# Kernel optimization log

Hardware: AMD Instinct MI355X
Metric: run time of the kernel (lower is better)

## Reference

```python
import jax, jax.numpy as jnp
import numpy as np

DIM = 1024
N_HEADS = 16
HEAD_DIM = DIM // N_HEADS
MLP = 4 * DIM
B, N = 2, 2048
LN_EPS = 1e-5


def setup_inputs() -> dict:
    key = jax.random.key(0)
    ks = jax.random.split(key, 12)
    s = lambda fan_in: 1.0 / np.sqrt(fan_in)
    return {
        "x": jax.random.normal(ks[0], (B, N, DIM), dtype=jnp.float32),
        "qkv_w": jax.random.uniform(ks[1], (3 * DIM, DIM), jnp.float32, -s(DIM), s(DIM)),
        "out_w": jax.random.uniform(ks[2], (DIM, DIM), jnp.float32, -s(DIM), s(DIM)),
        "out_b": jax.random.uniform(ks[3], (DIM,), jnp.float32, -s(DIM), s(DIM)),
        "ff_w1": jax.random.uniform(ks[4], (MLP, DIM), jnp.float32, -s(DIM), s(DIM)),
        "ff_b1": jax.random.uniform(ks[5], (MLP,), jnp.float32, -s(DIM), s(DIM)),
        "ff_w2": jax.random.uniform(ks[6], (DIM, MLP), jnp.float32, -s(MLP), s(MLP)),
        "ff_b2": jax.random.uniform(ks[7], (DIM,), jnp.float32, -s(MLP), s(MLP)),
        "ln1_w": jnp.ones((DIM,), jnp.float32),
        "ln1_b": jnp.zeros((DIM,), jnp.float32),
        "ln2_w": jnp.ones((DIM,), jnp.float32),
        "ln2_b": jnp.zeros((DIM,), jnp.float32),
    }


def _layernorm(x, w, b):
    mu = jnp.mean(x, axis=-1, keepdims=True)
    var = jnp.mean(jnp.square(x - mu), axis=-1, keepdims=True)
    return (x - mu) * jax.lax.rsqrt(var + LN_EPS) * w + b


def reference(x, qkv_w, out_w, out_b, ff_w1, ff_b1, ff_w2, ff_b2,
              ln1_w, ln1_b, ln2_w, ln2_b):
    Bx, Nx, D = x.shape
    scale = HEAD_DIM ** -0.5
    x_ln = _layernorm(x, ln1_w, ln1_b)
    qkv = (x_ln @ qkv_w.T).reshape(Bx, Nx, 3, N_HEADS, HEAD_DIM)
    qkv = jnp.transpose(qkv, (2, 0, 3, 1, 4))  # [3, B, H, N, hd]
    q, k, v = qkv[0], qkv[1], qkv[2]
    attn = jnp.einsum('bhid,bhjd->bhij', q, k) * scale
    attn = jax.nn.softmax(attn, axis=-1)
    o = jnp.einsum('bhij,bhjd->bhid', attn, v)
    o = jnp.transpose(o, (0, 2, 1, 3)).reshape(Bx, Nx, D)
    x = x + o @ out_w.T + out_b
    x_ln2 = _layernorm(x, ln2_w, ln2_b)
    h = jax.nn.silu(x_ln2 @ ff_w1.T + ff_b1)
    x = x + h @ ff_w2.T + ff_b2
    return x
```

## Files before the change

### kernel.cpp

```cpp
#include <hip/hip_runtime.h>
#include <stdint.h>

#define DIM   1024
#define NH    16
#define HD    64
#define SEQ   2048
#define BATCH 2
#define MROWS 4096
#define MLPD  4096
#define LN_EPS 1e-5f
#define QSCALE 0.18033688011112042f

typedef _Float16 f16;
typedef _Float16 half8 __attribute__((ext_vector_type(8)));
typedef _Float16 half4 __attribute__((ext_vector_type(4)));
typedef float f32x4 __attribute__((ext_vector_type(4)));

__device__ __forceinline__ void async_cp16(const void* g, void* l) {
  __builtin_amdgcn_global_load_lds(
      (const __attribute__((address_space(1))) unsigned int*)g,
      (__attribute__((address_space(3))) unsigned int*)l, 16, 0, 0);
}

__global__ __launch_bounds__(256) void cvt_all_kernel(
    const float* __restrict__ w0, const float* __restrict__ w1,
    const float* __restrict__ w2, const float* __restrict__ w3,
    f16* __restrict__ d0, f16* __restrict__ d1, f16* __restrict__ d2,
    f16* __restrict__ d3) {
  int blk = blockIdx.x;
  const float* s;
  f16* d;
  int base;
  if (blk < 3072)      { s = w0; d = d0; base = blk; }
  else if (blk < 4096) { s = w1; d = d1; base = blk - 3072; }
  else if (blk < 8192) { s = w2; d = d2; base = blk - 4096; }
  else                 { s = w3; d = d3; base = blk - 8192; }
  int i = (base * 256 + threadIdx.x) * 4;
  float4 v = *(const float4*)(s + i);
  half4 o = { (f16)v.x, (f16)v.y, (f16)v.z, (f16)v.w };
  *(half4*)(d + i) = o;
}

__global__ __launch_bounds__(256) void ln_kernel(const float* __restrict__ x,
    const float* __restrict__ w, const float* __restrict__ b, f16* __restrict__ out) {
  __shared__ float red[8];
  int row = blockIdx.x, t = threadIdx.x;
  const float4 v = ((const float4*)(x + (size_t)row * DIM))[t];
  float s1 = v.x + v.y + v.z + v.w;
  float s2 = v.x * v.x + v.y * v.y + v.z * v.z + v.w * v.w;
#pragma unroll
  for (int m = 32; m; m >>= 1) { s1 += __shfl_xor(s1, m); s2 += __shfl_xor(s2, m); }
  if ((t & 63) == 0) { red[t >> 6] = s1; red[4 + (t >> 6)] = s2; }
  __syncthreads();
  s1 = red[0] + red[1] + red[2] + red[3];
  s2 = red[4] + red[5] + red[6] + red[7];
  float mu = s1 * (1.f / DIM);
  float rs = rsqrtf(s2 * (1.f / DIM) - mu * mu + LN_EPS);
  float4 wv = ((const float4*)w)[t];
  float4 bv = ((const float4*)b)[t];
  half4 o = { (f16)((v.x - mu) * rs * wv.x + bv.x), (f16)((v.y - mu) * rs * wv.y + bv.y),
              (f16)((v.z - mu) * rs * wv.z + bv.z), (f16)((v.w - mu) * rs * wv.w + bv.w) };
  ((half4*)(out + (size_t)row * DIM))[t] = o;
}

template <int MODE, int TN>
__global__ __launch_bounds__(256) void gemm_bt(
    const f16* __restrict__ A, const f16* __restrict__ W,
    const float* __restrict__ bias, const float* __restrict__ resid,
    float* __restrict__ outf, f16* __restrict__ outq, f16* __restrict__ outk,
    f16* __restrict__ outv, int K) {
  constexpr int IT = (TN == 128) ? 4 : 2;
  constexpr int MSUB = IT * 16;
  __shared__ __align__(16) f16 As[128 * 64];
  __shared__ __align__(16) f16 Bs[TN * 64];
  const int t = threadIdx.x;
  const int wave = t >> 6, lane = t & 63;
  const int n16 = lane & 15, quad = lane >> 4;
  const int tile_m = blockIdx.y * 128, tile_n = blockIdx.x * TN;
  const int wm = (TN == 128) ? (wave >> 1) : wave;
  const int wn = (TN == 128) ? (wave & 1) : 0;
  const int srow = lane >> 3, spos = lane & 7;
  const f32x4 zero4 = {0.f, 0.f, 0.f, 0.f};

  f32x4 acc[IT][4];
#pragma unroll
  for (int i = 0; i < IT; i++)
#pragma unroll
    for (int j = 0; j < 4; j++) acc[i][j] = zero4;

  for (int k0 = 0; k0 < K; k0 += 64) {
#pragma unroll
    for (int q = 0; q < 4; q++) {
      int r = q * 32 + wave * 8 + srow;
      int c = spos ^ (r & 7);
      async_cp16(A + (size_t)(tile_m + r) * K + k0 + c * 8, &As[q * 2048 + wave * 512]);
    }
#pragma unroll
    for (int q = 0; q < TN / 32; q++) {
      int r = q * 32 + wave * 8 + srow;
      int c = spos ^ (r & 7);
      async_cp16(W + (size_t)(tile_n + r) * K + k0 + c * 8, &Bs[q * 2048 + wave * 512]);
    }
    __syncthreads();
#pragma unroll
    for (int kk = 0; kk < 2; kk++) {
      half8 af[IT], bfr[4];
#pragma unroll
      for (int i = 0; i < IT; i++) {
        int row = wm * MSUB + i * 16 + n16;
        int c = (kk * 4 + quad) ^ (row & 7);
        af[i] = *(const half8*)&As[row * 64 + c * 8];
      }
#pragma unroll
      for (int j = 0; j < 4; j++) {
        int row = wn * 64 + j * 16 + n16;
        int c = (kk * 4 + quad) ^ (row & 7);
        bfr[j] = *(const half8*)&Bs[row * 64 + c * 8];
      }
#pragma unroll
      for (int i = 0; i < IT; i++)
#pragma unroll
        for (int j = 0; j < 4; j++)
          acc[i][j] = __builtin_amdgcn_mfma_f32_16x16x32_f16(af[i], bfr[j], acc[i][j], 0, 0, 0);
    }
    __syncthreads();
  }

#pragma unroll
  for (int i = 0; i < IT; i++) {
#pragma unroll
    for (int j = 0; j < 4; j++) {
      int gcol = tile_n + wn * 64 + j * 16 + n16;
      int grow0 = tile_m + wm * MSUB + i * 16 + quad * 4;
      if constexpr (MODE == 0) {
        int tsel = gcol >> 10, h = (gcol >> 6) & 15, d = gcol & 63;
        int bb = grow0 >> 11, nn0 = grow0 & 2047;
        if (tsel == 2) {
          half4 o;
#pragma unroll
          for (int r = 0; r < 4; r++) o[r] = (f16)acc[i][j][r];
          *(half4*)&outv[(((size_t)bb * NH + h) * HD + d) * SEQ + nn0] = o;
        } else {
          f16* dst = (tsel == 0) ? outq : outk;
          float sc = (tsel == 0) ? QSCALE : 1.0f;
#pragma unroll
          for (int r = 0; r < 4; r++)
            dst[(((size_t)bb * NH + h) * SEQ + nn0 + r) * HD + d] = (f16)(acc[i][j][r] * sc);
        }
      } else if constexpr (MODE == 1) {
#pragma unroll
        for (int r = 0; r < 4; r++) {
          size_t idx = (size_t)(grow0 + r) * DIM + gcol;
          outf[idx] = acc[i][j][r] + bias[gcol] + resid[idx];
        }
      } else {
#pragma unroll
        for (int r = 0; r < 4; r++) {
          float z = acc[i][j][r] + bias[gcol];
          float sg = 1.f / (1.f + __expf(-z));
          outq[(size_t)(grow0 + r) * MLPD + gcol] = (f16)(z * sg);
        }
      }
    }
  }
}

__global__ __launch_bounds__(256, 4) void attn_kernel(const f16* __restrict__ qg,
    const f16* __restrict__ kg, const f16* __restrict__ vtg,
    float* __restrict__ op, float* __restrict__ lp) {
  __shared__ __align__(16) f16 Ks[64 * 64];
  __shared__ __align__(16) f16 Vs[64 * 64];
  const int bh = blockIdx.z, kc = blockIdx.y, q0 = blockIdx.x * 128;
  const int t = threadIdx.x, wave = t >> 6, lane = t & 63;
  const int n16 = lane & 15, quad = lane >> 4;
  const int srow = lane >> 3, spos = lane & 7;
  const f32x4 zero4 = {0.f, 0.f, 0.f, 0.f};

  half8 qf[2][2];
#pragma unroll
  for (int qt = 0; qt < 2; qt++) {
    const f16* qr = qg + ((size_t)bh * SEQ + q0 + wave * 32 + qt * 16 + n16) * HD + quad * 8;
    qf[qt][0] = *(const half8*)qr;
    qf[qt][1] = *(const half8*)(qr + 32);
  }

  f32x4 oc[2][4];
#pragma unroll
  for (int qt = 0; qt < 2; qt++)
#pragma unroll
    for (int dt = 0; dt < 4; dt++) oc[qt][dt] = zero4;
  float ls[2] = {0.f, 0.f};

  for (int kt64 = 0; kt64 < 16; kt64++) {
    const int kv0 = kc * 1024 + kt64 * 64;
#pragma unroll
    for (int p = 0; p < 2; p++) {
      int r = p * 32 + wave * 8 + srow;
      int c = spos ^ (r & 7);
      async_cp16(kg + ((size_t)bh * SEQ + kv0 + r) * HD + c * 8, &Ks[p * 2048 + wave * 512]);
      async_cp16(vtg + ((size_t)bh * HD + r) * SEQ + kv0 + c * 8, &Vs[p * 2048 + wave * 512]);
    }
    __syncthreads();

    f32x4 st[4][2];
#pragma unroll
    for (int kt = 0; kt < 4; kt++) {
      int row = kt * 16 + n16;
      half8 kf0 = *(const half8*)&Ks[row * 64 + (quad ^ (row & 7)) * 8];
      half8 kf1 = *(const half8*)&Ks[row * 64 + ((quad + 4) ^ (row & 7)) * 8];
#pragma unroll
      for (int qt = 0; qt < 2; qt++) {
        f32x4 z = zero4;
        z = __builtin_amdgcn_mfma_f32_16x16x32_f16(kf0, qf[qt][0], z, 0, 0, 0);
        z = __builtin_amdgcn_mfma_f32_16x16x32_f16(kf1, qf[qt][1], z, 0, 0, 0);
        st[kt][qt] = z;
      }
    }

    half4 pf[2][4];
#pragma unroll
    for (int qt = 0; qt < 2; qt++)
#pragma unroll
      for (int kt = 0; kt < 4; kt++) {
        half4 p4;
        float s0 = __builtin_exp2f(st[kt][qt][0]);
        float s1 = __builtin_exp2f(st[kt][qt][1]);
        float s2 = __builtin_exp2f(st[kt][qt][2]);
        float s3 = __builtin_exp2f(st[kt][qt][3]);
        p4[0] = (f16)s0; p4[1] = (f16)s1; p4[2] = (f16)s2; p4[3] = (f16)s3;
        ls[qt] += (s0 + s1) + (s2 + s3);
        pf[qt][kt] = p4;
      }

#pragma unroll
    for (int kt = 0; kt < 4; kt++) {
      half4 va[4];
#pragma unroll
      for (int dt = 0; dt < 4; dt++) {
        int row = dt * 16 + n16;
        int phys = (kt * 2 + (quad >> 1)) ^ (row & 7);
        va[dt] = *(const half4*)&Vs[row * 64 + phys * 8 + (quad & 1) * 4];
      }
#pragma unroll
      for (int dt = 0; dt < 4; dt++)
#pragma unroll
        for (int qt = 0; qt < 2; qt++)
          oc[qt][dt] = __builtin_amdgcn_mfma_f32_16x16x16f16(va[dt], pf[qt][kt], oc[qt][dt], 0, 0, 0);
    }
    __syncthreads();
  }

  const int b = bh >> 4, h = bh & 15;
#pragma unroll
  for (int qt = 0; qt < 2; qt++) {
    float l = ls[qt];
    l += __shfl_xor(l, 16);
    l += __shfl_xor(l, 32);
    int q = q0 + wave * 32 + qt * 16 + n16;
    int row = b * SEQ + q;
#pragma unroll
    for (int dt = 0; dt < 4; dt++)
      *(f32x4*)&op[((size_t)kc * MROWS + row) * DIM + h * HD + dt * 16 + quad * 4] = oc[qt][dt];
    if (quad == 0) lp[((size_t)kc * BATCH * NH + bh) * SEQ + q] = l;
  }
}

__global__ __launch_bounds__(256) void attn_reduce_kernel(const float* __restrict__ op,
    const float* __restrict__ lp, f16* __restrict__ obuf) {
  int row = blockIdx.x;
  int t = threadIdx.x;
  int b = row >> 11, q = row & 2047;
  int h = t >> 4;
  size_t base = (size_t)row * DIM + t * 4;
  float4 o1 = *(const float4*)&op[base];
  float4 o2 = *(const float4*)&op[(size_t)MROWS * DIM + base];
  size_t li = ((size_t)b * NH + h) * SEQ + q;
  float l = lp[li] + lp[(size_t)BATCH * NH * SEQ + li];
  float inv = 1.f / l;
  half4 o = { (f16)((o1.x + o2.x) * inv), (f16)((o1.y + o2.y) * inv),
              (f16)((o1.z + o2.z) * inv), (f16)((o1.w + o2.w) * inv) };
  *(half4*)&obuf[base] = o;
}

extern "C" void kernel_launch(void* const* d_in, const int* in_sizes, int n_in,
                              void* d_out, int out_size, void* d_ws, size_t ws_size,
                              hipStream_t stream) {
  const float* x     = (const float*)d_in[0];
  const float* qkv_w = (const float*)d_in[1];
  const float* out_w = (const float*)d_in[2];
  const float* out_b = (const float*)d_in[3];
  const float* ff_w1 = (const float*)d_in[4];
  const float* ff_b1 = (const float*)d_in[5];
  const float* ff_w2 = (const float*)d_in[6];
  const float* ff_b2 = (const float*)d_in[7];
  const float* ln1_w = (const float*)d_in[8];
  const float* ln1_b = (const float*)d_in[9];
  const float* ln2_w = (const float*)d_in[10];
  const float* ln2_b = (const float*)d_in[11];
  float* out = (float*)d_out;

  char* p = (char*)d_ws;
  size_t off = 0;
  auto alloc = [&](size_t bytes) {
    void* r = p + off;
    off += (bytes + 255) & ~(size_t)255;
    return r;
  };
  f16* wqkv = (f16*)alloc((size_t)3 * DIM * DIM * 2);
  f16* wout = (f16*)alloc((size_t)DIM * DIM * 2);
  f16* wf1  = (f16*)alloc((size_t)MLPD * DIM * 2);
  f16* wf2  = (f16*)alloc((size_t)MLPD * DIM * 2);
  f16* xln  = (f16*)alloc((size_t)MROWS * DIM * 2);
  f16* qb   = (f16*)alloc((size_t)MROWS * DIM * 2);
  f16* kb   = (f16*)alloc((size_t)MROWS * DIM * 2);
  f16* vtb  = (f16*)alloc((size_t)MROWS * DIM * 2);
  f16* obuf = (f16*)alloc((size_t)MROWS * DIM * 2);
  float* x1 = (float*)alloc((size_t)MROWS * DIM * 4);
  f16* hbuf = (f16*)alloc((size_t)MROWS * MLPD * 2);
  float* lp = (float*)alloc((size_t)2 * BATCH * NH * SEQ * 4);
  f16* x1ln = xln;
  float* op = (float*)hbuf;

  cvt_all_kernel<<<12288, 256, 0, stream>>>(qkv_w, out_w, ff_w1, ff_w2,
                                            wqkv, wout, wf1, wf2);
  ln_kernel<<<MROWS, 256, 0, stream>>>(x, ln1_w, ln1_b, xln);
  gemm_bt<0, 128><<<dim3(3 * DIM / 128, MROWS / 128), 256, 0, stream>>>(
      xln, wqkv, nullptr, nullptr, nullptr, qb, kb, vtb, DIM);
  attn_kernel<<<dim3(SEQ / 128, 2, BATCH * NH), 256, 0, stream>>>(qb, kb, vtb, op, lp);
  attn_reduce_kernel<<<MROWS, 256, 0, stream>>>(op, lp, obuf);
  gemm_bt<1, 64><<<dim3(DIM / 64, MROWS / 128), 256, 0, stream>>>(
      obuf, wout, out_b, x, x1, nullptr, nullptr, nullptr, DIM);
  ln_kernel<<<MROWS, 256, 0, stream>>>(x1, ln2_w, ln2_b, x1ln);
  gemm_bt<2, 128><<<dim3(MLPD / 128, MROWS / 128), 256, 0, stream>>>(
      x1ln, wf1, ff_b1, nullptr, nullptr, hbuf, nullptr, nullptr, DIM);
  gemm_bt<1, 64><<<dim3(DIM / 64, MROWS / 128), 256, 0, stream>>>(
      hbuf, wf2, ff_b2, x1, out, nullptr, nullptr, nullptr, MLPD);
}
```

Baseline: 364.5 us.

## Split-K the N=1024 GEMMs and fuse bias/residual/LN2 into combine kernels

The out-projection and FF2 GEMMs are split along K into two halves via a third grid dimension, writing fp32 partials into reused scratch buffers. New combine kernels sum the partials with bias and residual, and the first also computes LayerNorm2, replacing the separate LN kernel. This doubles the block count for the narrow GEMMs to fill more CUs, at the cost of extra fp32 partial traffic and an added launch. Launch bounds for TN=64 request higher occupancy.

```diff
diff --git a/kernel.cpp b/kernel.cpp
--- a/kernel.cpp
+++ b/kernel.cpp
@@ -64,11 +64,11 @@
 }
 
 template <int MODE, int TN>
-__global__ __launch_bounds__(256) void gemm_bt(
+__global__ __launch_bounds__(256, (TN == 64) ? 4 : 1) void gemm_bt(
     const f16* __restrict__ A, const f16* __restrict__ W,
-    const float* __restrict__ bias, const float* __restrict__ resid,
-    float* __restrict__ outf, f16* __restrict__ outq, f16* __restrict__ outk,
-    f16* __restrict__ outv, int K) {
+    const float* __restrict__ bias, float* __restrict__ outf,
+    f16* __restrict__ outq, f16* __restrict__ outk, f16* __restrict__ outv,
+    int K) {
   constexpr int IT = (TN == 128) ? 4 : 2;
   constexpr int MSUB = IT * 16;
   __shared__ __align__(16) f16 As[128 * 64];
@@ -82,13 +82,20 @@
   const int srow = lane >> 3, spos = lane & 7;
   const f32x4 zero4 = {0.f, 0.f, 0.f, 0.f};
 
+  int kbeg = 0, kend = K;
+  if constexpr (MODE == 3) {
+    int kc = K >> 1;
+    kbeg = blockIdx.z * kc;
+    kend = kbeg + kc;
+  }
+
   f32x4 acc[IT][4];
 #pragma unroll
   for (int i = 0; i < IT; i++)
 #pragma unroll
     for (int j = 0; j < 4; j++) acc[i][j] = zero4;
 
-  for (int k0 = 0; k0 < K; k0 += 64) {
+  for (int k0 = kbeg; k0 < kend; k0 += 64) {
 #pragma unroll
     for (int q = 0; q < 4; q++) {
       int r = q * 32 + wave * 8 + srow;
@@ -147,12 +154,10 @@
           for (int r = 0; r < 4; r++)
             dst[(((size_t)bb * NH + h) * SEQ + nn0 + r) * HD + d] = (f16)(acc[i][j][r] * sc);
         }
-      } else if constexpr (MODE == 1) {
-#pragma unroll
-        for (int r = 0; r < 4; r++) {
-          size_t idx = (size_t)(grow0 + r) * DIM + gcol;
-          outf[idx] = acc[i][j][r] + bias[gcol] + resid[idx];
-        }
+      } else if constexpr (MODE == 3) {
+        size_t base = ((size_t)blockIdx.z * MROWS + grow0) * DIM + gcol;
+#pragma unroll
+        for (int r = 0; r < 4; r++) outf[base + (size_t)r * DIM] = acc[i][j][r];
       } else {
 #pragma unroll
         for (int r = 0; r < 4; r++) {
@@ -163,6 +168,51 @@
       }
     }
   }
+}
+
+__global__ __launch_bounds__(256) void combine_ln_kernel(const float* __restrict__ op,
+    const float* __restrict__ bias, const float* __restrict__ resid,
+    const float* __restrict__ lnw, const float* __restrict__ lnb,
+    float* __restrict__ x1, f16* __restrict__ x1ln) {
+  __shared__ float red[8];
+  int row = blockIdx.x, t = threadIdx.x;
+  size_t base = (size_t)row * DIM;
+  float4 p0 = ((const float4*)&op[base])[t];
+  float4 p1 = ((const float4*)&op[(size_t)MROWS * DIM + base])[t];
+  float4 bv = ((const float4*)bias)[t];
+  float4 rv = ((const float4*)&resid[base])[t];
+  float4 v = { p0.x + p1.x + bv.x + rv.x, p0.y + p1.y + bv.y + rv.y,
+               p0.z + p1.z + bv.z + rv.z, p0.w + p1.w + bv.w + rv.w };
+  ((float4*)&x1[base])[t] = v;
+  float s1 = v.x + v.y + v.z + v.w;
+  float s2 = v.x * v.x + v.y * v.y + v.z * v.z + v.w * v.w;
+#pragma unroll
+  for (int m = 32; m; m >>= 1) { s1 += __shfl_xor(s1, m); s2 += __shfl_xor(s2, m); }
+  if ((t & 63) == 0) { red[t >> 6] = s1; red[4 + (t >> 6)] = s2; }
+  __syncthreads();
+  s1 = red[0] + red[1] + red[2] + red[3];
+  s2 = red[4] + red[5] + red[6] + red[7];
+  float mu = s1 * (1.f / DIM);
+  float rs = rsqrtf(s2 * (1.f / DIM) - mu * mu + LN_EPS);
+  float4 wv = ((const float4*)lnw)[t];
+  float4 lb = ((const float4*)lnb)[t];
+  half4 o = { (f16)((v.x - mu) * rs * wv.x + lb.x), (f16)((v.y - mu) * rs * wv.y + lb.y),
+              (f16)((v.z - mu) * rs * wv.z + lb.z), (f16)((v.w - mu) * rs * wv.w + lb.w) };
+  ((half4*)&x1ln[base])[t] = o;
+}
+
+__global__ __launch_bounds__(256) void combine_out_kernel(const float* __restrict__ op,
+    const float* __restrict__ bias, const float* __restrict__ resid,
+    float* __restrict__ out) {
+  int row = blockIdx.x, t = threadIdx.x;
+  size_t base = (size_t)row * DIM;
+  float4 p0 = ((const float4*)&op[base])[t];
+  float4 p1 = ((const float4*)&op[(size_t)MROWS * DIM + base])[t];
+  float4 bv = ((const float4*)bias)[t];
+  float4 rv = ((const float4*)&resid[base])[t];
+  float4 v = { p0.x + p1.x + bv.x + rv.x, p0.y + p1.y + bv.y + rv.y,
+               p0.z + p1.z + bv.z + rv.z, p0.w + p1.w + bv.w + rv.w };
+  ((float4*)&out[base])[t] = v;
 }
 
 __global__ __launch_bounds__(256, 4) void attn_kernel(const f16* __restrict__ qg,
@@ -319,20 +369,23 @@
   f16* hbuf = (f16*)alloc((size_t)MROWS * MLPD * 2);
   float* lp = (float*)alloc((size_t)2 * BATCH * NH * SEQ * 4);
   f16* x1ln = xln;
-  float* op = (float*)hbuf;
+  float* opa = (float*)hbuf;
+  float* op1 = (float*)hbuf;
+  float* op2 = (float*)qb;
 
   cvt_all_kernel<<<12288, 256, 0, stream>>>(qkv_w, out_w, ff_w1, ff_w2,
                                             wqkv, wout, wf1, wf2);
   ln_kernel<<<MROWS, 256, 0, stream>>>(x, ln1_w, ln1_b, xln);
   gemm_bt<0, 128><<<dim3(3 * DIM / 128, MROWS / 128), 256, 0, stream>>>(
-      xln, wqkv, nullptr, nullptr, nullptr, qb, kb, vtb, DIM);
-  attn_kernel<<<dim3(SEQ / 128, 2, BATCH * NH), 256, 0, stream>>>(qb, kb, vtb, op, lp);
-  attn_reduce_kernel<<<MROWS, 256, 0, stream>>>(op, lp, obuf);
-  gemm_bt<1, 64><<<dim3(DIM / 64, MROWS / 128), 256, 0, stream>>>(
-      obuf, wout, out_b, x, x1, nullptr, nullptr, nullptr, DIM);
-  ln_kernel<<<MROWS, 256, 0, stream>>>(x1, ln2_w, ln2_b, x1ln);
+      xln, wqkv, nullptr, nullptr, qb, kb, vtb, DIM);
+  attn_kernel<<<dim3(SEQ / 128, 2, BATCH * NH), 256, 0, stream>>>(qb, kb, vtb, opa, lp);
+  attn_reduce_kernel<<<MROWS, 256, 0, stream>>>(opa, lp, obuf);
+  gemm_bt<3, 64><<<dim3(DIM / 64, MROWS / 128, 2), 256, 0, stream>>>(
+      obuf, wout, nullptr, op1, nullptr, nullptr, nullptr, DIM);
+  combine_ln_kernel<<<MROWS, 256, 0, stream>>>(op1, out_b, x, ln2_w, ln2_b, x1, x1ln);
   gemm_bt<2, 128><<<dim3(MLPD / 128, MROWS / 128), 256, 0, stream>>>(
-      x1ln, wf1, ff_b1, nullptr, nullptr, hbuf, nullptr, nullptr, DIM);
-  gemm_bt<1, 64><<<dim3(DIM / 64, MROWS / 128), 256, 0, stream>>>(
-      hbuf, wf2, ff_b2, x1, out, nullptr, nullptr, nullptr, MLPD);
-}
+      x1ln, wf1, ff_b1, nullptr, hbuf, nullptr, nullptr, DIM);
+  gemm_bt<3, 64><<<dim3(DIM / 64, MROWS / 128, 2), 256, 0, stream>>>(
+      hbuf, wf2, nullptr, op2, nullptr, nullptr, nullptr, MLPD);
+  combine_out_kernel<<<MROWS, 256, 0, stream>>>(op2, ff_b2, x1, out);
+}
```

After: 365.0 us. About the same (+0.1%).

## Shrink output-projection GEMM tiles to 64x64 and double attention KV tile per barrier

Applied to the files above, without the earlier changes.

The GEMM template gains a TM parameter, and the two DIM-wide output GEMMs now use 64x64 tiles with a launch bound of 4 blocks per SM, doubling grid size so more CUs are busy on these narrow GEMMs. The attention kernel now loads 128 keys per iteration into two LDS sub-buffers and processes both before syncing, halving barrier and load-issue rounds. The cost is more LDS per attention block, which may reduce occupancy, and lower data reuse per block in the smaller GEMM tiles.

```diff
diff --git a/kernel.cpp b/kernel.cpp
--- a/kernel.cpp
+++ b/kernel.cpp
@@ -63,20 +63,20 @@
   ((half4*)(out + (size_t)row * DIM))[t] = o;
 }
 
-template <int MODE, int TN>
-__global__ __launch_bounds__(256) void gemm_bt(
+template <int MODE, int TM, int TN>
+__global__ __launch_bounds__(256, (TN == 64) ? 4 : 1) void gemm_bt(
     const f16* __restrict__ A, const f16* __restrict__ W,
     const float* __restrict__ bias, const float* __restrict__ resid,
     float* __restrict__ outf, f16* __restrict__ outq, f16* __restrict__ outk,
     f16* __restrict__ outv, int K) {
-  constexpr int IT = (TN == 128) ? 4 : 2;
+  constexpr int IT = (TN == 128) ? (TM / 32) : (TM / 64);
   constexpr int MSUB = IT * 16;
-  __shared__ __align__(16) f16 As[128 * 64];
+  __shared__ __align__(16) f16 As[TM * 64];
   __shared__ __align__(16) f16 Bs[TN * 64];
   const int t = threadIdx.x;
   const int wave = t >> 6, lane = t & 63;
   const int n16 = lane & 15, quad = lane >> 4;
-  const int tile_m = blockIdx.y * 128, tile_n = blockIdx.x * TN;
+  const int tile_m = blockIdx.y * TM, tile_n = blockIdx.x * TN;
   const int wm = (TN == 128) ? (wave >> 1) : wave;
   const int wn = (TN == 128) ? (wave & 1) : 0;
   const int srow = lane >> 3, spos = lane & 7;
@@ -90,7 +90,7 @@
 
   for (int k0 = 0; k0 < K; k0 += 64) {
 #pragma unroll
-    for (int q = 0; q < 4; q++) {
+    for (int q = 0; q < TM / 32; q++) {
       int r = q * 32 + wave * 8 + srow;
       int c = spos ^ (r & 7);
       async_cp16(A + (size_t)(tile_m + r) * K + k0 + c * 8, &As[q * 2048 + wave * 512]);
@@ -168,8 +168,8 @@
 __global__ __launch_bounds__(256, 4) void attn_kernel(const f16* __restrict__ qg,
     const f16* __restrict__ kg, const f16* __restrict__ vtg,
     float* __restrict__ op, float* __restrict__ lp) {
-  __shared__ __align__(16) f16 Ks[64 * 64];
-  __shared__ __align__(16) f16 Vs[64 * 64];
+  __shared__ __align__(16) f16 Ks[2][64 * 64];
+  __shared__ __align__(16) f16 Vs[2][64 * 64];
   const int bh = blockIdx.z, kc = blockIdx.y, q0 = blockIdx.x * 128;
   const int t = threadIdx.x, wave = t >> 6, lane = t & 63;
   const int n16 = lane & 15, quad = lane >> 4;
@@ -191,61 +191,68 @@
     for (int dt = 0; dt < 4; dt++) oc[qt][dt] = zero4;
   float ls[2] = {0.f, 0.f};
 
-  for (int kt64 = 0; kt64 < 16; kt64++) {
-    const int kv0 = kc * 1024 + kt64 * 64;
-#pragma unroll
-    for (int p = 0; p < 2; p++) {
-      int r = p * 32 + wave * 8 + srow;
-      int c = spos ^ (r & 7);
-      async_cp16(kg + ((size_t)bh * SEQ + kv0 + r) * HD + c * 8, &Ks[p * 2048 + wave * 512]);
-      async_cp16(vtg + ((size_t)bh * HD + r) * SEQ + kv0 + c * 8, &Vs[p * 2048 + wave * 512]);
-    }
+  for (int kt128 = 0; kt128 < 8; kt128++) {
+    const int kv0 = kc * 1024 + kt128 * 128;
+#pragma unroll
+    for (int sub = 0; sub < 2; sub++)
+#pragma unroll
+      for (int p = 0; p < 2; p++) {
+        int r = p * 32 + wave * 8 + srow;
+        int c = spos ^ (r & 7);
+        async_cp16(kg + ((size_t)bh * SEQ + kv0 + sub * 64 + r) * HD + c * 8,
+                   &Ks[sub][p * 2048 + wave * 512]);
+        async_cp16(vtg + ((size_t)bh * HD + r) * SEQ + kv0 + sub * 64 + c * 8,
+                   &Vs[sub][p * 2048 + wave * 512]);
+      }
     __syncthreads();
 
-    f32x4 st[4][2];
-#pragma unroll
-    for (int kt = 0; kt < 4; kt++) {
-      int row = kt * 16 + n16;
-      half8 kf0 = *(const half8*)&Ks[row * 64 + (quad ^ (row & 7)) * 8];
-      half8 kf1 = *(const half8*)&Ks[row * 64 + ((quad + 4) ^ (row & 7)) * 8];
-#pragma unroll
-      for (int qt = 0; qt < 2; qt++) {
-        f32x4 z = zero4;
-        z = __builtin_amdgcn_mfma_f32_16x16x32_f16(kf0, qf[qt][0], z, 0, 0, 0);
-        z = __builtin_amdgcn_mfma_f32_16x16x32_f16(kf1, qf[qt][1], z, 0, 0, 0);
-        st[kt][qt] = z;
-      }
-    }
-
-    half4 pf[2][4];
-#pragma unroll
-    for (int qt = 0; qt < 2; qt++)
+#pragma unroll
+    for (int sub = 0; sub < 2; sub++) {
+      f32x4 st[4][2];
 #pragma unroll
       for (int kt = 0; kt < 4; kt++) {
-        half4 p4;
-        float s0 = __builtin_exp2f(st[kt][qt][0]);
-        float s1 = __builtin_exp2f(st[kt][qt][1]);
-        float s2 = __builtin_exp2f(st[kt][qt][2]);
-        float s3 = __builtin_exp2f(st[kt][qt][3]);
-        p4[0] = (f16)s0; p4[1] = (f16)s1; p4[2] = (f16)s2; p4[3] = (f16)s3;
-        ls[qt] += (s0 + s1) + (s2 + s3);
-        pf[qt][kt] = p4;
-      }
-
-#pragma unroll
-    for (int kt = 0; kt < 4; kt++) {
-      half4 va[4];
-#pragma unroll
-      for (int dt = 0; dt < 4; dt++) {
-        int row = dt * 16 + n16;
-        int phys = (kt * 2 + (quad >> 1)) ^ (row & 7);
-        va[dt] = *(const half4*)&Vs[row * 64 + phys * 8 + (quad & 1) * 4];
-      }
-#pragma unroll
-      for (int dt = 0; dt < 4; dt++)
-#pragma unroll
-        for (int qt = 0; qt < 2; qt++)
-          oc[qt][dt] = __builtin_amdgcn_mfma_f32_16x16x16f16(va[dt], pf[qt][kt], oc[qt][dt], 0, 0, 0);
+        int row = kt * 16 + n16;
+        half8 kf0 = *(const half8*)&Ks[sub][row * 64 + (quad ^ (row & 7)) * 8];
+        half8 kf1 = *(const half8*)&Ks[sub][row * 64 + ((quad + 4) ^ (row & 7)) * 8];
+#pragma unroll
+        for (int qt = 0; qt < 2; qt++) {
+          f32x4 z = zero4;
+          z = __builtin_amdgcn_mfma_f32_16x16x32_f16(kf0, qf[qt][0], z, 0, 0, 0);
+          z = __builtin_amdgcn_mfma_f32_16x16x32_f16(kf1, qf[qt][1], z, 0, 0, 0);
+          st[kt][qt] = z;
+        }
+      }
+
+      half4 pf[2][4];
+#pragma unroll
+      for (int qt = 0; qt < 2; qt++)
+#pragma unroll
+        for (int kt = 0; kt < 4; kt++) {
+          half4 p4;
+          float s0 = __builtin_exp2f(st[kt][qt][0]);
+          float s1 = __builtin_exp2f(st[kt][qt][1]);
+          float s2 = __builtin_exp2f(st[kt][qt][2]);
+          float s3 = __builtin_exp2f(st[kt][qt][3]);
+          p4[0] = (f16)s0; p4[1] = (f16)s1; p4[2] = (f16)s2; p4[3] = (f16)s3;
+          ls[qt] += (s0 + s1) + (s2 + s3);
+          pf[qt][kt] = p4;
+        }
+
+#pragma unroll
+      for (int kt = 0; kt < 4; kt++) {
+        half4 va[4];
+#pragma unroll
+        for (int dt = 0; dt < 4; dt++) {
+          int row = dt * 16 + n16;
+          int phys = (kt * 2 + (quad >> 1)) ^ (row & 7);
+          va[dt] = *(const half4*)&Vs[sub][row * 64 + phys * 8 + (quad & 1) * 4];
+        }
+#pragma unroll
+        for (int dt = 0; dt < 4; dt++)
+#pragma unroll
+          for (int qt = 0; qt < 2; qt++)
+            oc[qt][dt] = __builtin_amdgcn_mfma_f32_16x16x16f16(va[dt], pf[qt][kt], oc[qt][dt], 0, 0, 0);
+      }
     }
     __syncthreads();
   }
@@ -319,20 +326,20 @@
   f16* hbuf = (f16*)alloc((size_t)MROWS * MLPD * 2);
   float* lp = (float*)alloc((size_t)2 * BATCH * NH * SEQ * 4);
   f16* x1ln = xln;
-  float* op = (float*)hbuf;
+  float* opa = (float*)hbuf;
 
   cvt_all_kernel<<<12288, 256, 0, stream>>>(qkv_w, out_w, ff_w1, ff_w2,
                                             wqkv, wout, wf1, wf2);
   ln_kernel<<<MROWS, 256, 0, stream>>>(x, ln1_w, ln1_b, xln);
-  gemm_bt<0, 128><<<dim3(3 * DIM / 128, MROWS / 128), 256, 0, stream>>>(
+  gemm_bt<0, 128, 128><<<dim3(3 * DIM / 128, MROWS / 128), 256, 0, stream>>>(
       xln, wqkv, nullptr, nullptr, nullptr, qb, kb, vtb, DIM);
-  attn_kernel<<<dim3(SEQ / 128, 2, BATCH * NH), 256, 0, stream>>>(qb, kb, vtb, op, lp);
-  attn_reduce_kernel<<<MROWS, 256, 0, stream>>>(op, lp, obuf);
-  gemm_bt<1, 64><<<dim3(DIM / 64, MROWS / 128), 256, 0, stream>>>(
+  attn_kernel<<<dim3(SEQ / 128, 2, BATCH * NH), 256, 0, stream>>>(qb, kb, vtb, opa, lp);
+  attn_reduce_kernel<<<MROWS, 256, 0, stream>>>(opa, lp, obuf);
+  gemm_bt<1, 64, 64><<<dim3(DIM / 64, MROWS / 64), 256, 0, stream>>>(
       obuf, wout, out_b, x, x1, nullptr, nullptr, nullptr, DIM);
   ln_kernel<<<MROWS, 256, 0, stream>>>(x1, ln2_w, ln2_b, x1ln);
-  gemm_bt<2, 128><<<dim3(MLPD / 128, MROWS / 128), 256, 0, stream>>>(
+  gemm_bt<2, 128, 128><<<dim3(MLPD / 128, MROWS / 128), 256, 0, stream>>>(
       x1ln, wf1, ff_b1, nullptr, nullptr, hbuf, nullptr, nullptr, DIM);
-  gemm_bt<1, 64><<<dim3(DIM / 64, MROWS / 128), 256, 0, stream>>>(
+  gemm_bt<1, 64, 64><<<dim3(DIM / 64, MROWS / 64), 256, 0, stream>>>(
       hbuf, wf2, ff_b2, x1, out, nullptr, nullptr, nullptr, MLPD);
 }
```

New measurement: 416.8 us. +14.3%, slower.
